# Kernel optimization log

Measured on AMD Instinct MI355X. Metric: run time of the kernel, lower is better.

Reference implementation:

```python
import jax, jax.numpy as jnp
import numpy as np

B, T, D, H = 4096, 100, 64, 128
N_RK4 = 4  # fixed RK4 substeps per observation gap (deterministic stand-in for adaptive odeint)


def setup_inputs() -> dict:
    key = jax.random.key(0)
    ks = jax.random.split(key, 12)
    x_seq = jax.random.normal(ks[0], (B, T, D), dtype=jnp.float32)
    # strictly increasing shared timestamps (source only uses t_seq[0, :])
    t0 = jnp.cumsum(jax.random.uniform(ks[1], (T,), dtype=jnp.float32) * 0.1 + 0.01)
    t_seq = jnp.broadcast_to(t0, (B, T))
    s_h = 1.0 / np.sqrt(H)
    s_d = 1.0 / np.sqrt(D)
    # ODE func: f(h) = tanh(h W1^T + b1) W2^T + b2
    W1 = jax.random.normal(ks[2], (H, H), jnp.float32) * s_h
    b1 = jnp.zeros((H,), jnp.float32)
    W2 = jax.random.normal(ks[3], (H, H), jnp.float32) * s_h * 0.1
    b2 = jnp.zeros((H,), jnp.float32)
    # GRUCell params (PyTorch layout: [3H, in])
    W_ih = jax.random.normal(ks[4], (3 * H, D), jnp.float32) * s_d
    W_hh = jax.random.normal(ks[5], (3 * H, H), jnp.float32) * s_h
    b_ih = jax.random.normal(ks[6], (3 * H,), jnp.float32) * s_h
    b_hh = jax.random.normal(ks[7], (3 * H,), jnp.float32) * s_h
    W_mu = jax.random.normal(ks[8], (H, H), jnp.float32) * s_h
    b_mu = jnp.zeros((H,), jnp.float32)
    W_lv = jax.random.normal(ks[9], (H, H), jnp.float32) * s_h
    b_lv = jnp.zeros((H,), jnp.float32)
    return dict(x_seq=x_seq, t_seq=t_seq, W1=W1, b1=b1, W2=W2, b2=b2,
                W_ih=W_ih, W_hh=W_hh, b_ih=b_ih, b_hh=b_hh,
                W_mu=W_mu, b_mu=b_mu, W_lv=W_lv, b_lv=b_lv)


def _odernn(x_seq, t_seq, W1, b1, W2, b2, W_ih, W_hh, b_ih, b_hh, W_mu, b_mu, W_lv, b_lv):
    Hdim = W1.shape[0]

    def f(h):  # ode_func, autonomous
        return jnp.tanh(h @ W1.T + b1) @ W2.T + b2

    def rk4_jump(h, dt):  # integrate dh/dt = f(h) over dt with N_RK4 substeps
        sub = dt / N_RK4  # scalar
        for _ in range(N_RK4):
            k1 = f(h)
            k2 = f(h + 0.5 * sub * k1)
            k3 = f(h + 0.5 * sub * k2)
            k4 = f(h + sub * k3)
            h = h + (sub / 6.0) * (k1 + 2.0 * k2 + 2.0 * k3 + k4)
        return h

    def gru(x, h):
        gi = x @ W_ih.T + b_ih  # [B, 3H]
        gh = h @ W_hh.T + b_hh
        i_r, i_z, i_n = jnp.split(gi, 3, axis=-1)
        h_r, h_z, h_n = jnp.split(gh, 3, axis=-1)
        r = jax.nn.sigmoid(i_r + h_r)
        z = jax.nn.sigmoid(i_z + h_z)
        n = jnp.tanh(i_n + r * h_n)
        return (1.0 - z) * n + z * h

    t0 = t_seq[0]  # [T] shared times, as in source (t_seq[0, i])
    dt = jnp.concatenate([jnp.zeros((1,), t0.dtype), t0[1:] - t0[:-1]])  # dt[0]=0 -> no jump at i=0
    h0 = jnp.zeros((x_seq.shape[0], Hdim), x_seq.dtype)

    def step(h, inp):
        x_i, dt_i = inp
        h = rk4_jump(h, dt_i)
        h = gru(x_i, h)
        return h, None

    h, _ = jax.lax.scan(step, h0, (jnp.swapaxes(x_seq, 0, 1), dt))
    mu = h @ W_mu.T + b_mu
    logvar = h @ W_lv.T + b_lv
    return mu, logvar


def reference(x_seq, t_seq, W1, b1, W2, b2, W_ih, W_hh, b_ih, b_hh, W_mu, b_mu, W_lv, b_lv):
    return _odernn(x_seq, t_seq, W1, b1, W2, b2, W_ih, W_hh, b_ih, b_hh, W_mu, b_mu, W_lv, b_lv)
```

## Files before the change

kernel.cpp:

```cpp
#include <hip/hip_runtime.h>

#define Bn 4096
#define Tn 100
#define Dn 64
#define Hn 128

typedef _Float16 half8v __attribute__((ext_vector_type(8)));
typedef _Float16 half4v __attribute__((ext_vector_type(4)));
typedef float    float4v __attribute__((ext_vector_type(4)));
typedef float    float2v __attribute__((ext_vector_type(2)));
typedef long     long2v  __attribute__((ext_vector_type(2)));

__device__ __forceinline__ float fast_tanh(float x) {
    float e = __expf(x + x);
    return 1.0f - 2.0f * __builtin_amdgcn_rcpf(e + 1.0f);
}
__device__ __forceinline__ float fast_sig(float x) {
    return __builtin_amdgcn_rcpf(1.0f + __expf(-x));
}
__device__ __forceinline__ float4v tanh4(float4v u) {
    float4v a;
#pragma unroll
    for (int r = 0; r < 4; r++) a[r] = fast_tanh(u[r]);
    return a;
}
__device__ __forceinline__ half4v pack4(float4v v) {
    half4v p;
#pragma unroll
    for (int r = 0; r < 4; r++) p[r] = (_Float16)v[r];
    return p;
}
__device__ __forceinline__ int pack_fp8x4(float a, float b, float c, float d) {
    int v = __builtin_amdgcn_cvt_pk_fp8_f32(a, b, 0, false);
    v = __builtin_amdgcn_cvt_pk_fp8_f32(c, d, v, true);
    return v;
}
__device__ __forceinline__ long pack_fp8x8s(float4v a, float4v b, float s) {
    int lo = pack_fp8x4(a[0]*s, a[1]*s, a[2]*s, a[3]*s);
    int hi = pack_fp8x4(b[0]*s, b[1]*s, b[2]*s, b[3]*s);
    return (long)(((unsigned long long)(unsigned)hi << 32) | (unsigned)lo);
}

__device__ __forceinline__ half8v load_wfrag(const float* __restrict__ W, int ld, int n, int k) {
    const float* p = W + (size_t)n * ld + k;
    float4v a = *(const float4v*)p;
    float4v b = *(const float4v*)(p + 4);
    half8v r;
    r[0] = (_Float16)a[0]; r[1] = (_Float16)a[1]; r[2] = (_Float16)a[2]; r[3] = (_Float16)a[3];
    r[4] = (_Float16)b[0]; r[5] = (_Float16)b[1]; r[6] = (_Float16)b[2]; r[7] = (_Float16)b[3];
    return r;
}

__global__ __launch_bounds__(512) void odernn_kernel(
    const float* __restrict__ x_seq, const float* __restrict__ t_seq,
    const float* __restrict__ W1,   const float* __restrict__ b1,
    const float* __restrict__ W2,   const float* __restrict__ b2,
    const float* __restrict__ W_ih, const float* __restrict__ W_hh,
    const float* __restrict__ b_ih, const float* __restrict__ b_hh,
    const float* __restrict__ W_mu, const float* __restrict__ b_mu,
    const float* __restrict__ W_lv, const float* __restrict__ b_lv,
    float* __restrict__ out)
{
    __shared__ _Float16 vbuf[16 * 136];
    __shared__ __attribute__((aligned(16))) unsigned char abuf8[2][16 * 144];
    __shared__ _Float16 xbuf[16 * 72];
    __shared__ float    ts_l[Tn];
    __shared__ float    c1s[Hn];

    const int tid  = threadIdx.x;
    const int lane = tid & 63;
    const int w    = tid >> 6;
    const int q    = lane >> 4;
    const int m    = lane & 15;
    const int blk  = blockIdx.x;

    if (tid < Tn) ts_l[tid] = t_seq[tid];
    for (int i = tid; i < 16 * 136; i += 512) vbuf[i] = (_Float16)0.f;
    if (tid < Hn) {
        float acc = 0.f;
        const float* r1 = W1 + (size_t)tid * Hn;
#pragma unroll 4
        for (int j = 0; j < Hn; j++) acc += b2[j] * r1[j];
        c1s[tid] = acc;
    }

    const int n0 = 16 * w + m;
    half8v w1f[4], whhf[3][4], wihf[3][2];
#pragma unroll
    for (int kt = 0; kt < 4; kt++) w1f[kt] = load_wfrag(W1, Hn, n0, 32 * kt + q * 8);
#pragma unroll
    for (int g = 0; g < 3; g++) {
        int n = 128 * g + n0;
#pragma unroll
        for (int kt = 0; kt < 4; kt++) whhf[g][kt] = load_wfrag(W_hh, Hn, n, 32 * kt + q * 8);
#pragma unroll
        for (int kt = 0; kt < 2; kt++) wihf[g][kt] = load_wfrag(W_ih, Dn, n, 32 * kt + q * 8);
    }
    float4v b1q = *(const float4v*)(b1 + 16 * w + q * 4);
    float4v b2q = *(const float4v*)(b2 + 16 * w + q * 4);
    float4v bihq[3], bhhq[3];
#pragma unroll
    for (int g = 0; g < 3; g++) {
        bihq[g] = *(const float4v*)(b_ih + 128 * g + 16 * w + q * 4);
        bhhq[g] = *(const float4v*)(b_hh + 128 * g + 16 * w + q * 4);
    }

    float4v aM[4][2];
#pragma unroll
    for (int kt = 0; kt < 4; kt++) {
        float4v zz = {0.f, 0.f, 0.f, 0.f};
        aM[kt][0] = zz; aM[kt][1] = zz;
    }
    {
        const float* w1row = W1 + (size_t)n0 * Hn;
        for (int j = 0; j < Hn; j++) {
            float w1v = w1row[j];
            const float* w2r = W2 + (size_t)j * Hn + q * 8;
#pragma unroll
            for (int kt = 0; kt < 4; kt++) {
                aM[kt][0] += w1v * *(const float4v*)(w2r + 32 * kt);
                aM[kt][1] += w1v * *(const float4v*)(w2r + 32 * kt + 4);
            }
        }
    }
    long w21f8[4], w2f8[4];
#pragma unroll
    for (int kt = 0; kt < 4; kt++) {
        w21f8[kt] = pack_fp8x8s(aM[kt][0], aM[kt][1], 64.0f);
        const float* p = W2 + (size_t)n0 * Hn + 32 * kt + q * 8;
        w2f8[kt] = pack_fp8x8s(*(const float4v*)p, *(const float4v*)(p + 4), 64.0f);
    }

    float4v h = {0.f, 0.f, 0.f, 0.f};

    const int xrow = tid >> 5;
    const int xcol = (tid & 31) * 2;
    const float* xptr = x_seq + (size_t)(blk * 16 + xrow) * (Tn * Dn) + xcol;
    float2v xreg = *(const float2v*)xptr;

    const int wslot = m * 136 + 16 * w + q * 4;
    const int ppos = 64 * (w >> 2) + 16 * ((2 * (w & 3) + (q >> 1)) & 3)
                   + 8 * ((w >> 1) & 1) + 4 * (q & 1);
    const float4v zero4 = {0.f, 0.f, 0.f, 0.f};

    auto store_a = [&](int pp, float4v v) {
        *(int*)(abuf8[pp] + m * 144 + ppos) = pack_fp8x4(v[0], v[1], v[2], v[3]);
    };
    auto gemm8 = [&](const long* Wf, int pp) -> float4v {
        const unsigned char* p = abuf8[pp] + m * 144;
        long2v L0 = *(const long2v*)(p + q * 16);
        long2v L1 = *(const long2v*)(p + 64 + q * 16);
        float4v o1 = zero4, o2 = zero4;
        o1 = __builtin_amdgcn_mfma_f32_16x16x32_fp8_fp8(Wf[0], L0[0], o1, 0, 0, 0);
        o2 = __builtin_amdgcn_mfma_f32_16x16x32_fp8_fp8(Wf[2], L1[0], o2, 0, 0, 0);
        o1 = __builtin_amdgcn_mfma_f32_16x16x32_fp8_fp8(Wf[1], L0[1], o1, 0, 0, 0);
        o2 = __builtin_amdgcn_mfma_f32_16x16x32_fp8_fp8(Wf[3], L1[1], o2, 0, 0, 0);
        return o1 + o2;
    };

    float4v c1q;
    __syncthreads();
#pragma unroll
    for (int r = 0; r < 4; r++) c1q[r] = c1s[16 * w + q * 4 + r];

#pragma unroll 1
    for (int t = 0; t < Tn; ++t) {
        {
            _Float16* xp = xbuf + xrow * 72 + xcol;
            xp[0] = (_Float16)xreg[0]; xp[1] = (_Float16)xreg[1];
        }
        float tc   = ts_l[t];
        float tp   = (t > 0) ? ts_l[t - 1] : tc;
        float sub  = (tc - tp) * 0.25f;
        float hs   = 0.5f * sub;
        float s6   = sub * (1.0f / 6.0f);
        float hs64 = hs * (1.0f / 64.0f);
        float sb64 = sub * (1.0f / 64.0f);
        float s664 = s6 * (1.0f / 64.0f);
        __syncthreads();
        if (t + 1 < Tn) xreg = *(const float2v*)(xptr + (t + 1) * Dn);

        float4v gi[3], u_h;
        {
            const _Float16* xp = xbuf + m * 72 + q * 8;
            half8v xf0 = *(const half8v*)(xp);
            half8v xf1 = *(const half8v*)(xp + 32);
#pragma unroll
            for (int g = 0; g < 3; g++) {
                float4v acc = bihq[g];
                acc = __builtin_amdgcn_mfma_f32_16x16x32_f16(wihf[g][0], xf0, acc, 0, 0, 0);
                acc = __builtin_amdgcn_mfma_f32_16x16x32_f16(wihf[g][1], xf1, acc, 0, 0, 0);
                gi[g] = acc;
            }
            const _Float16* vp = vbuf + m * 136 + q * 8;
            half8v bf0 = *(const half8v*)(vp);
            half8v bf1 = *(const half8v*)(vp + 32);
            half8v bf2 = *(const half8v*)(vp + 64);
            half8v bf3 = *(const half8v*)(vp + 96);
            float4v o1 = b1q, o2 = zero4;
            o1 = __builtin_amdgcn_mfma_f32_16x16x32_f16(w1f[0], bf0, o1, 0, 0, 0);
            o2 = __builtin_amdgcn_mfma_f32_16x16x32_f16(w1f[2], bf2, o2, 0, 0, 0);
            o1 = __builtin_amdgcn_mfma_f32_16x16x32_f16(w1f[1], bf1, o1, 0, 0, 0);
            o2 = __builtin_amdgcn_mfma_f32_16x16x32_f16(w1f[3], bf3, o2, 0, 0, 0);
            u_h = o1 + o2;
        }

        if (sub != 0.0f) {
            float4v Abar = zero4;
#pragma unroll 1
            for (int s = 0; s < 4; s++) {
                float4v a1 = tanh4(u_h);
                float4v A = a1;
                store_a(0, a1);
                __syncthreads();
                float4v g = gemm8(w21f8, 0);
                float4v u = u_h + hs64 * g + hs * c1q;
                float4v a2 = tanh4(u);
                A += 2.0f * a2;
                store_a(1, a2);
                __syncthreads();
                g = gemm8(w21f8, 1);
                u = u_h + hs64 * g + hs * c1q;
                float4v a3 = tanh4(u);
                A += 2.0f * a3;
                store_a(0, a3);
                __syncthreads();
                g = gemm8(w21f8, 0);
                u = u_h + sb64 * g + sub * c1q;
                float4v a4 = tanh4(u);
                A += a4;
                Abar += A;
                if (s < 3) {
                    store_a(1, A);
                    __syncthreads();
                    g = gemm8(w21f8, 1);
                    u_h += s664 * g + sub * c1q;
                }
            }
            store_a(1, Abar);
            __syncthreads();
            float4v gw = gemm8(w2f8, 1);
            h += s664 * gw + (4.0f * sub) * b2q;
            *(half4v*)(vbuf + wslot) = pack4(h);
            __syncthreads();
        }

        float4v gh[3];
        {
            const _Float16* vp = vbuf + m * 136 + q * 8;
            half8v bf0 = *(const half8v*)(vp);
            half8v bf1 = *(const half8v*)(vp + 32);
            half8v bf2 = *(const half8v*)(vp + 64);
            half8v bf3 = *(const half8v*)(vp + 96);
#pragma unroll
            for (int g = 0; g < 3; g++) {
                float4v acc = bhhq[g];
                acc = __builtin_amdgcn_mfma_f32_16x16x32_f16(whhf[g][0], bf0, acc, 0, 0, 0);
                acc = __builtin_amdgcn_mfma_f32_16x16x32_f16(whhf[g][1], bf1, acc, 0, 0, 0);
                acc = __builtin_amdgcn_mfma_f32_16x16x32_f16(whhf[g][2], bf2, acc, 0, 0, 0);
                acc = __builtin_amdgcn_mfma_f32_16x16x32_f16(whhf[g][3], bf3, acc, 0, 0, 0);
                gh[g] = acc;
            }
        }
        __syncthreads();

        {
            half4v pk;
#pragma unroll
            for (int r = 0; r < 4; r++) {
                float rr = fast_sig(gi[0][r] + gh[0][r]);
                float zz = fast_sig(gi[1][r] + gh[1][r]);
                float nn = fast_tanh(gi[2][r] + rr * gh[2][r]);
                float hv = (1.0f - zz) * nn + zz * h[r];
                h[r] = hv;
                pk[r] = (_Float16)hv;
            }
            *(half4v*)(vbuf + wslot) = pk;
        }
    }

    __syncthreads();

#pragma unroll
    for (int mat = 0; mat < 2; mat++) {
        const float* Wm = mat ? W_lv : W_mu;
        const float* bm = mat ? b_lv : b_mu;
        float4v acc = *(const float4v*)(bm + 16 * w + q * 4);
        const _Float16* p = vbuf + m * 136 + q * 8;
#pragma unroll
        for (int kt = 0; kt < 4; kt++) {
            half8v af = load_wfrag(Wm, Hn, n0, 32 * kt + q * 8);
            acc = __builtin_amdgcn_mfma_f32_16x16x32_f16(af, *(const half8v*)(p + kt * 32), acc, 0, 0, 0);
        }
        *(float4v*)(out + (size_t)mat * Bn * Hn + (size_t)(blk * 16 + m) * Hn + 16 * w + q * 4) = acc;
    }
}

extern "C" void kernel_launch(void* const* d_in, const int* in_sizes, int n_in,
                              void* d_out, int out_size, void* d_ws, size_t ws_size,
                              hipStream_t stream) {
    (void)in_sizes; (void)n_in; (void)d_ws; (void)ws_size; (void)out_size;
    odernn_kernel<<<dim3(Bn / 16), dim3(512), 0, stream>>>(
        (const float*)d_in[0],  (const float*)d_in[1],  (const float*)d_in[2],
        (const float*)d_in[3],  (const float*)d_in[4],  (const float*)d_in[5],
        (const float*)d_in[6],  (const float*)d_in[7],  (const float*)d_in[8],
        (const float*)d_in[9],  (const float*)d_in[10], (const float*)d_in[11],
        (const float*)d_in[12], (const float*)d_in[13], (float*)d_out);
}
```

Before: 883.6 us.

## Move W_ih fragments and biases to LDS, async-load x directly to LDS, force 2 waves/EU

The W_ih MFMA fragments and all bias vectors move from registers into shared memory (biases stored as fp16). The per-step x tile is loaded with global_load_lds straight into an fp32 LDS buffer. The input-gate GEMM moves from the start of the step to after the ODE jump, and waves_per_eu is pinned to 2. The goal is lower register pressure and more overlap of the x fetch with compute, at the cost of extra LDS reads each step and fp16 rounding of the biases.

```diff
diff --git a/kernel.cpp b/kernel.cpp
--- a/kernel.cpp
+++ b/kernel.cpp
@@ -5,11 +5,13 @@
 #define Dn 64
 #define Hn 128
 
-typedef _Float16 half8v __attribute__((ext_vector_type(8)));
-typedef _Float16 half4v __attribute__((ext_vector_type(4)));
+typedef _Float16 half8v  __attribute__((ext_vector_type(8)));
+typedef _Float16 half4v  __attribute__((ext_vector_type(4)));
 typedef float    float4v __attribute__((ext_vector_type(4)));
-typedef float    float2v __attribute__((ext_vector_type(2)));
 typedef long     long2v  __attribute__((ext_vector_type(2)));
+
+typedef __attribute__((address_space(1))) const unsigned int gu32;
+typedef __attribute__((address_space(3))) unsigned int       lu32;
 
 __device__ __forceinline__ float fast_tanh(float x) {
     float e = __expf(x + x);
@@ -29,6 +31,12 @@
 #pragma unroll
     for (int r = 0; r < 4; r++) p[r] = (_Float16)v[r];
     return p;
+}
+__device__ __forceinline__ float4v cvt4(half4v h) {
+    float4v f;
+#pragma unroll
+    for (int r = 0; r < 4; r++) f[r] = (float)h[r];
+    return f;
 }
 __device__ __forceinline__ int pack_fp8x4(float a, float b, float c, float d) {
     int v = __builtin_amdgcn_cvt_pk_fp8_f32(a, b, 0, false);
@@ -51,7 +59,8 @@
     return r;
 }
 
-__global__ __launch_bounds__(512) void odernn_kernel(
+__global__ __attribute__((amdgpu_flat_work_group_size(512, 512), amdgpu_waves_per_eu(2, 2)))
+void odernn_kernel(
     const float* __restrict__ x_seq, const float* __restrict__ t_seq,
     const float* __restrict__ W1,   const float* __restrict__ b1,
     const float* __restrict__ W2,   const float* __restrict__ b2,
@@ -61,11 +70,12 @@
     const float* __restrict__ W_lv, const float* __restrict__ b_lv,
     float* __restrict__ out)
 {
+    __shared__ float    ts_l[Tn];
     __shared__ _Float16 vbuf[16 * 136];
     __shared__ __attribute__((aligned(16))) unsigned char abuf8[2][16 * 144];
-    __shared__ _Float16 xbuf[16 * 72];
-    __shared__ float    ts_l[Tn];
-    __shared__ float    c1s[Hn];
+    __shared__ __attribute__((aligned(16))) float xbuf[16 * 68];
+    __shared__ _Float16 wih_l[8 * 6 * 64 * 8];
+    __shared__ _Float16 bias_l[1024];
 
     const int tid  = threadIdx.x;
     const int lane = tid & 63;
@@ -76,6 +86,15 @@
 
     if (tid < Tn) ts_l[tid] = t_seq[tid];
     for (int i = tid; i < 16 * 136; i += 512) vbuf[i] = (_Float16)0.f;
+    for (int i = tid; i < 1024; i += 512) {
+        float v;
+        if (i < 128) v = b1[i];
+        else if (i < 256) v = b2[i - 128];
+        else if (i < 640) v = b_ih[i - 256];
+        else v = b_hh[i - 640];
+        bias_l[i] = (_Float16)v;
+    }
+    float* c1s = (float*)abuf8[0];
     if (tid < Hn) {
         float acc = 0.f;
         const float* r1 = W1 + (size_t)tid * Hn;
@@ -83,27 +102,22 @@
         for (int j = 0; j < Hn; j++) acc += b2[j] * r1[j];
         c1s[tid] = acc;
     }
+#pragma unroll
+    for (int f = 0; f < 6; f++) {
+        int g = f >> 1, kt = f & 1;
+        half8v fr = load_wfrag(W_ih, Dn, 128 * g + 16 * w + m, 32 * kt + q * 8);
+        *(half8v*)(wih_l + ((w * 6 + f) * 64 + lane) * 8) = fr;
+    }
 
     const int n0 = 16 * w + m;
-    half8v w1f[4], whhf[3][4], wihf[3][2];
+    half8v w1f[4], whhf[3][4];
 #pragma unroll
     for (int kt = 0; kt < 4; kt++) w1f[kt] = load_wfrag(W1, Hn, n0, 32 * kt + q * 8);
 #pragma unroll
-    for (int g = 0; g < 3; g++) {
-        int n = 128 * g + n0;
-#pragma unroll
-        for (int kt = 0; kt < 4; kt++) whhf[g][kt] = load_wfrag(W_hh, Hn, n, 32 * kt + q * 8);
-#pragma unroll
-        for (int kt = 0; kt < 2; kt++) wihf[g][kt] = load_wfrag(W_ih, Dn, n, 32 * kt + q * 8);
-    }
-    float4v b1q = *(const float4v*)(b1 + 16 * w + q * 4);
-    float4v b2q = *(const float4v*)(b2 + 16 * w + q * 4);
-    float4v bihq[3], bhhq[3];
-#pragma unroll
-    for (int g = 0; g < 3; g++) {
-        bihq[g] = *(const float4v*)(b_ih + 128 * g + 16 * w + q * 4);
-        bhhq[g] = *(const float4v*)(b_hh + 128 * g + 16 * w + q * 4);
-    }
+    for (int g = 0; g < 3; g++)
+#pragma unroll
+        for (int kt = 0; kt < 4; kt++)
+            whhf[g][kt] = load_wfrag(W_hh, Hn, 128 * g + n0, 32 * kt + q * 8);
 
     float4v aM[4][2];
 #pragma unroll
@@ -132,16 +146,11 @@
     }
 
     float4v h = {0.f, 0.f, 0.f, 0.f};
-
-    const int xrow = tid >> 5;
-    const int xcol = (tid & 31) * 2;
-    const float* xptr = x_seq + (size_t)(blk * 16 + xrow) * (Tn * Dn) + xcol;
-    float2v xreg = *(const float2v*)xptr;
+    const float4v zero4 = {0.f, 0.f, 0.f, 0.f};
 
     const int wslot = m * 136 + 16 * w + q * 4;
     const int ppos = 64 * (w >> 2) + 16 * ((2 * (w & 3) + (q >> 1)) & 3)
                    + 8 * ((w >> 1) & 1) + 4 * (q & 1);
-    const float4v zero4 = {0.f, 0.f, 0.f, 0.f};
 
     auto store_a = [&](int pp, float4v v) {
         *(int*)(abuf8[pp] + m * 144 + ppos) = pack_fp8x4(v[0], v[1], v[2], v[3]);
@@ -157,47 +166,42 @@
         o2 = __builtin_amdgcn_mfma_f32_16x16x32_fp8_fp8(Wf[3], L1[1], o2, 0, 0, 0);
         return o1 + o2;
     };
-
+    const float* xbase = x_seq + (size_t)(blk * 16) * (Tn * Dn);
+    auto load_x = [&](int t) {
+#pragma unroll
+        for (int i = 0; i < 2; i++) {
+            int row = 2 * w + i;
+            const float* gp = xbase + ((size_t)row * Tn + t) * Dn + lane;
+            __builtin_amdgcn_global_load_lds((gu32*)gp, (lu32*)(xbuf + row * 68), 4, 0, 0);
+        }
+    };
+
+    load_x(0);
+    __syncthreads();
     float4v c1q;
-    __syncthreads();
 #pragma unroll
     for (int r = 0; r < 4; r++) c1q[r] = c1s[16 * w + q * 4 + r];
 
 #pragma unroll 1
     for (int t = 0; t < Tn; ++t) {
-        {
-            _Float16* xp = xbuf + xrow * 72 + xcol;
-            xp[0] = (_Float16)xreg[0]; xp[1] = (_Float16)xreg[1];
-        }
         float tc   = ts_l[t];
         float tp   = (t > 0) ? ts_l[t - 1] : tc;
         float sub  = (tc - tp) * 0.25f;
         float hs   = 0.5f * sub;
-        float s6   = sub * (1.0f / 6.0f);
         float hs64 = hs * (1.0f / 64.0f);
         float sb64 = sub * (1.0f / 64.0f);
-        float s664 = s6 * (1.0f / 64.0f);
+        float s664 = sub * (1.0f / 384.0f);
         __syncthreads();
-        if (t + 1 < Tn) xreg = *(const float2v*)(xptr + (t + 1) * Dn);
-
-        float4v gi[3], u_h;
+
+        float4v u_h;
         {
-            const _Float16* xp = xbuf + m * 72 + q * 8;
-            half8v xf0 = *(const half8v*)(xp);
-            half8v xf1 = *(const half8v*)(xp + 32);
-#pragma unroll
-            for (int g = 0; g < 3; g++) {
-                float4v acc = bihq[g];
-                acc = __builtin_amdgcn_mfma_f32_16x16x32_f16(wihf[g][0], xf0, acc, 0, 0, 0);
-                acc = __builtin_amdgcn_mfma_f32_16x16x32_f16(wihf[g][1], xf1, acc, 0, 0, 0);
-                gi[g] = acc;
-            }
             const _Float16* vp = vbuf + m * 136 + q * 8;
             half8v bf0 = *(const half8v*)(vp);
             half8v bf1 = *(const half8v*)(vp + 32);
             half8v bf2 = *(const half8v*)(vp + 64);
             half8v bf3 = *(const half8v*)(vp + 96);
-            float4v o1 = b1q, o2 = zero4;
+            float4v o1 = cvt4(*(const half4v*)(bias_l + 16 * w + q * 4));
+            float4v o2 = zero4;
             o1 = __builtin_amdgcn_mfma_f32_16x16x32_f16(w1f[0], bf0, o1, 0, 0, 0);
             o2 = __builtin_amdgcn_mfma_f32_16x16x32_f16(w1f[2], bf2, o2, 0, 0, 0);
             o1 = __builtin_amdgcn_mfma_f32_16x16x32_f16(w1f[1], bf1, o1, 0, 0, 0);
@@ -240,26 +244,45 @@
             store_a(1, Abar);
             __syncthreads();
             float4v gw = gemm8(w2f8, 1);
-            h += s664 * gw + (4.0f * sub) * b2q;
+            h += s664 * gw + (4.0f * sub) * cvt4(*(const half4v*)(bias_l + 128 + 16 * w + q * 4));
             *(half4v*)(vbuf + wslot) = pack4(h);
             __syncthreads();
         }
 
-        float4v gh[3];
+        float4v gh[3], gi[3];
         {
             const _Float16* vp = vbuf + m * 136 + q * 8;
             half8v bf0 = *(const half8v*)(vp);
             half8v bf1 = *(const half8v*)(vp + 32);
             half8v bf2 = *(const half8v*)(vp + 64);
             half8v bf3 = *(const half8v*)(vp + 96);
+            const float* xr = xbuf + m * 68;
+            half8v xf[2];
+#pragma unroll
+            for (int kt = 0; kt < 2; kt++) {
+                float4v xa = *(const float4v*)(xr + 32 * kt + q * 8);
+                float4v xb = *(const float4v*)(xr + 32 * kt + q * 8 + 4);
+#pragma unroll
+                for (int r = 0; r < 4; r++) {
+                    xf[kt][r]     = (_Float16)xa[r];
+                    xf[kt][r + 4] = (_Float16)xb[r];
+                }
+            }
 #pragma unroll
             for (int g = 0; g < 3; g++) {
-                float4v acc = bhhq[g];
+                float4v acc = cvt4(*(const half4v*)(bias_l + 640 + 128 * g + 16 * w + q * 4));
                 acc = __builtin_amdgcn_mfma_f32_16x16x32_f16(whhf[g][0], bf0, acc, 0, 0, 0);
                 acc = __builtin_amdgcn_mfma_f32_16x16x32_f16(whhf[g][1], bf1, acc, 0, 0, 0);
                 acc = __builtin_amdgcn_mfma_f32_16x16x32_f16(whhf[g][2], bf2, acc, 0, 0, 0);
                 acc = __builtin_amdgcn_mfma_f32_16x16x32_f16(whhf[g][3], bf3, acc, 0, 0, 0);
                 gh[g] = acc;
+                float4v acg = cvt4(*(const half4v*)(bias_l + 256 + 128 * g + 16 * w + q * 4));
+#pragma unroll
+                for (int kt = 0; kt < 2; kt++) {
+                    half8v wf = *(const half8v*)(wih_l + ((w * 6 + g * 2 + kt) * 64 + lane) * 8);
+                    acg = __builtin_amdgcn_mfma_f32_16x16x32_f16(wf, xf[kt], acg, 0, 0, 0);
+                }
+                gi[g] = acg;
             }
         }
         __syncthreads();
@@ -277,6 +300,7 @@
             }
             *(half4v*)(vbuf + wslot) = pk;
         }
+        if (t + 1 < Tn) load_x(t + 1);
     }
 
     __syncthreads();
```

Result: slower. 947.1 us (+7.2%).
